# Performance work log

Measured on AMD Instinct MI355X. Metric: run time of the kernel, lower is better.

Reference implementation:

```python
import jax, jax.numpy as jnp
import numpy as np
import math

B, IN, OUT = 1024, 512, 512


def setup_inputs() -> dict:
    key = jax.random.key(0)
    ks = jax.random.split(key, 7)
    std = 1.0 / math.sqrt(IN)
    x = jax.random.normal(ks[0], (B, IN), dtype=jnp.float32)
    base_weight = jax.random.uniform(ks[1], (OUT, IN), dtype=jnp.float32, minval=-std, maxval=std)
    chirplet_weights = jax.random.uniform(ks[2], (OUT, IN), dtype=jnp.float32, minval=-std, maxval=std)
    # scale init ones, frequency ones, translation zeros; add small jitter for a non-degenerate test point
    scale = 1.0 + 0.1 * jax.random.normal(ks[3], (OUT, IN), dtype=jnp.float32)
    translation = 0.1 * jax.random.normal(ks[4], (OUT, IN), dtype=jnp.float32)
    frequency = 1.0 + 0.1 * jax.random.normal(ks[5], (OUT, IN), dtype=jnp.float32)
    bias = jax.random.uniform(ks[6], (OUT,), dtype=jnp.float32, minval=-std, maxval=std)
    return {"x": x, "base_weight": base_weight, "chirplet_weights": chirplet_weights,
            "scale": scale, "translation": translation, "frequency": frequency, "bias": bias}


def reference(x, base_weight, chirplet_weights, scale, translation, frequency, bias):
    TWO_PI = 2.0 * math.pi
    # base linear path: SiLU(x) @ W^T
    base_out = jnp.einsum('bi,oi->bo', jax.nn.silu(x), base_weight)
    # chirplet path: (b, o, i) intermediate reduced over i
    x_scaled = (x[:, None, :] - translation[None, :, :]) / scale[None, :, :]  # (B, OUT, IN)
    chirplet = jnp.cos(TWO_PI * frequency[None, :, :] * x_scaled) * jnp.exp(-0.5 * x_scaled ** 2)
    chirplet_out = jnp.einsum('boi,oi->bo', chirplet, chirplet_weights)
    return base_out + chirplet_out + bias[None, :]
```

## Files before the change

kernel.cpp:

```cpp
#include <hip/hip_runtime.h>
#include <hip/hip_bf16.h>

#define B_ 1024
#define IN_ 512
#define OUT_ 512
#define BTILE 64
#define OTILE 32
#define ITILE 8
#define KSPLIT 16
#define KCHUNK (IN_ / KSPLIT)
#define NCHUNKS (KCHUNK / ITILE)
#define P4STRIDE 128
#define PLSTRIDE 32
#define XSTRIDE 68
#define ASTRIDE 40

typedef float v2f   __attribute__((ext_vector_type(2)));
typedef float f32x4 __attribute__((ext_vector_type(4)));
typedef short s16x8 __attribute__((ext_vector_type(8)));
#define PKFMA(a, b, c) __builtin_elementwise_fma((v2f)(a), (v2f)(b), (v2f)(c))

__device__ __forceinline__ unsigned short f2bf(float f) {
    union { float f; unsigned int u; } v; v.f = f;
    unsigned int b = v.u + 0x7FFFu + ((v.u >> 16) & 1u);
    return (unsigned short)(b >> 16);
}
__device__ __forceinline__ float fast_exp2(float x) {
#if __has_builtin(__builtin_amdgcn_exp2f)
    return __builtin_amdgcn_exp2f(x);
#else
    return __exp2f(x);
#endif
}
__device__ __forceinline__ float fast_log2(float x) {
#if __has_builtin(__builtin_amdgcn_logf)
    return __builtin_amdgcn_logf(x);
#else
    return __log2f(x);
#endif
}
__device__ __forceinline__ float fast_cos_rev(float x) {
#if __has_builtin(__builtin_amdgcn_cosf)
    return __builtin_amdgcn_cosf(x);
#else
    return __cosf(x * 6.2831853071795864f);
#endif
}
__device__ __forceinline__ float fast_rcp(float x) {
#if __has_builtin(__builtin_amdgcn_rcpf)
    return __builtin_amdgcn_rcpf(x);
#else
    return 1.0f / x;
#endif
}

__global__ __launch_bounds__(256, 8) void chirplet_kernel(
    const float* __restrict__ x,
    const float* __restrict__ W,
    const float* __restrict__ Wc,
    const float* __restrict__ S,
    const float* __restrict__ T,
    const float* __restrict__ F,
    const float* __restrict__ bias,
    float* __restrict__ out)
{
    __shared__ __align__(16) float p4_lds[ITILE * P4STRIDE];
    __shared__ __align__(16) float plw_lds[ITILE * PLSTRIDE];
    __shared__ __align__(16) float x_lds[ITILE * XSTRIDE];
    __shared__ __align__(16) unsigned short sA_lds[BTILE * ASTRIDE];
    __shared__ __align__(16) unsigned short wB_lds[OTILE * ASTRIDE];

    const int tid  = threadIdx.x;
    const int wave = tid >> 6;
    const int lane = tid & 63;
    const int o0 = blockIdx.x * OTILE;
    const int b0 = blockIdx.y * BTILE;
    const int k0 = blockIdx.z * KCHUNK;

    const int oc = tid & 15;
    const int bq = tid >> 4;

    const int xrow = tid >> 2;
    const int xq   = tid & 3;

    const int pol = tid & 31;
    const int pi  = tid >> 5;

    const float LOG2E = 1.4426950408889634f;
    const float GK    = 0.8493218002880191f;

    v2f acc2[2][2] = {{{0.f,0.f},{0.f,0.f}},{{0.f,0.f},{0.f,0.f}}};

    for (int c = 0; c < NCHUNKS; ++c) {
        const int ib = k0 + c * ITILE;

        {
            const float2 v = *(const float2*)(x + (size_t)(b0 + xrow) * IN_ + ib + xq * 2);
            const float xf[2] = { v.x, v.y };
            unsigned int packed = 0;
            #pragma unroll
            for (int j = 0; j < 2; ++j) {
                const int col = xq * 2 + j;
                float xv  = xf[j];
                float sig = fast_rcp(1.0f + fast_exp2(-xv * LOG2E));
                x_lds[col * XSTRIDE + xrow] = xv;
                packed |= (unsigned int)f2bf(xv * sig) << (16 * j);
            }
            *(unsigned int*)&sA_lds[xrow * ASTRIDE + c * 8 + xq * 2] = packed;
        }

        {
            const size_t go = (size_t)(o0 + pol) * IN_ + ib + pi;
            const float s  = S[go];
            const float t  = T[go];
            const float f  = F[go];
            const float w  = W[go];
            const float wc = Wc[go];
            const float rs = fast_rcp(s);
            const float a  = f * rs;
            float4 p0;
            p0.x = a;
            p0.y = -a * t + (wc < 0.0f ? 0.5f : 0.0f);
            p0.z = rs * GK;
            p0.w = -t * rs * GK;
            *(float4*)&p4_lds[pi * P4STRIDE + pol * 4] = p0;
            plw_lds[pi * PLSTRIDE + pol] = fast_log2(fabsf(wc));
            wB_lds[pol * ASTRIDE + c * 8 + pi] = f2bf(w);
        }
        __syncthreads();

        #pragma unroll 4
        for (int i = 0; i < ITILE; ++i) {
            const float4 abcd[2] = {
                *(const float4*)&p4_lds[i * P4STRIDE + oc * 4],
                *(const float4*)&p4_lds[i * P4STRIDE + (oc + 16) * 4] };
            const float lw[2] = {
                plw_lds[i * PLSTRIDE + oc],
                plw_lds[i * PLSTRIDE + oc + 16] };
            const v2f* xp = (const v2f*)&x_lds[i * XSTRIDE + bq * 4];
            const v2f xk2[2] = { xp[0], xp[1] };
            #pragma unroll
            for (int o = 0; o < 2; ++o) {
                const v2f aa = { abcd[o].x, abcd[o].x };
                const v2f bb = { abcd[o].y, abcd[o].y };
                const v2f cc = { abcd[o].z, abcd[o].z };
                const v2f dd = { abcd[o].w, abcd[o].w };
                const v2f lwv = { lw[o], lw[o] };
                #pragma unroll
                for (int p = 0; p < 2; ++p) {
                    v2f rev = PKFMA(aa, xk2[p], bb);
                    v2f u   = PKFMA(cc, xk2[p], dd);
                    v2f arg = PKFMA(-u, u, lwv);
                    v2f co, e;
                    co.x = fast_cos_rev(rev.x);
                    co.y = fast_cos_rev(rev.y);
                    e.x  = fast_exp2(arg.x);
                    e.y  = fast_exp2(arg.y);
                    acc2[o][p] = PKFMA(co, e, acc2[o][p]);
                }
            }
        }
        __syncthreads();
    }

    const int q8 = (lane >> 4) * 8;
    const s16x8 af  = *(const s16x8*)&sA_lds[(wave * 16 + (lane & 15)) * ASTRIDE + q8];
    const s16x8 bf0 = *(const s16x8*)&wB_lds[(lane & 15) * ASTRIDE + q8];
    const s16x8 bf1 = *(const s16x8*)&wB_lds[((lane & 15) + 16) * ASTRIDE + q8];
    const f32x4 mz = { 0.f, 0.f, 0.f, 0.f };
    const f32x4 m0 = __builtin_amdgcn_mfma_f32_16x16x32_bf16(af, bf0, mz, 0, 0, 0);
    const f32x4 m1 = __builtin_amdgcn_mfma_f32_16x16x32_bf16(af, bf1, mz, 0, 0, 0);

    const float badd[2] = { (blockIdx.z == 0) ? bias[o0 + oc] : 0.0f,
                            (blockIdx.z == 0) ? bias[o0 + oc + 16] : 0.0f };
    #pragma unroll
    for (int o = 0; o < 2; ++o) {
        #pragma unroll
        for (int p = 0; p < 2; ++p) {
            #pragma unroll
            for (int j = 0; j < 2; ++j) {
                const int reg = p * 2 + j;
                const int b = b0 + bq * 4 + reg;
                float* dst = &out[(size_t)b * OUT_ + o0 + oc + o * 16];
                const float mm = (o == 0) ? m0[reg] : m1[reg];
                const float val = (j == 0 ? acc2[o][p].x : acc2[o][p].y) + mm + badd[o];
#if defined(__HIP_DEVICE_COMPILE__)
                unsafeAtomicAdd(dst, val);
#else
                atomicAdd(dst, val);
#endif
            }
        }
    }
}

extern "C" void kernel_launch(void* const* d_in, const int* in_sizes, int n_in,
                              void* d_out, int out_size, void* d_ws, size_t ws_size,
                              hipStream_t stream) {
    const float* x    = (const float*)d_in[0];
    const float* W    = (const float*)d_in[1];
    const float* Wc   = (const float*)d_in[2];
    const float* S    = (const float*)d_in[3];
    const float* T    = (const float*)d_in[4];
    const float* F    = (const float*)d_in[5];
    const float* bias = (const float*)d_in[6];
    float* out = (float*)d_out;

    hipMemsetAsync(out, 0, (size_t)out_size * sizeof(float), stream);

    dim3 grid(OUT_ / OTILE, B_ / BTILE, KSPLIT);
    chirplet_kernel<<<grid, 256, 0, stream>>>(x, W, Wc, S, T, F, bias, out);
}
```

Baseline: 125.9 us.

## Shrink blocks to 128 threads, halve K-split, accumulate MFMA per chunk

Blocks shrink from 64x32 to 32x32 (batch x output) with 128 threads, and the K-split drops from 16 to 8, so each block walks twice as many input chunks. The base-path bf16 MFMA now runs once per 8-wide chunk into a running accumulator, with only the first 16 lanes loading data and the rest fed zeros. Parameter loads are widened to float2, and LDS row strides are padded. The aim is to halve the atomic adds to the output and reuse the parameter transforms across more of the batch. The cost is fewer, longer blocks and an MFMA issued with most of its K dimension padded with zeros on every chunk.

```diff
diff --git a/kernel.cpp b/kernel.cpp
--- a/kernel.cpp
+++ b/kernel.cpp
@@ -4,16 +4,17 @@
 #define B_ 1024
 #define IN_ 512
 #define OUT_ 512
-#define BTILE 64
+#define BTILE 32
 #define OTILE 32
 #define ITILE 8
-#define KSPLIT 16
+#define KSPLIT 8
 #define KCHUNK (IN_ / KSPLIT)
 #define NCHUNKS (KCHUNK / ITILE)
-#define P4STRIDE 128
-#define PLSTRIDE 32
-#define XSTRIDE 68
-#define ASTRIDE 40
+#define THREADS 128
+#define P4ROW 132
+#define PLROW 33
+#define XSTRIDE 36
+#define SASTRIDE 8
 
 typedef float v2f   __attribute__((ext_vector_type(2)));
 typedef float f32x4 __attribute__((ext_vector_type(4)));
@@ -54,7 +55,7 @@
 #endif
 }
 
-__global__ __launch_bounds__(256, 8) void chirplet_kernel(
+__global__ __launch_bounds__(THREADS, 8) void chirplet_kernel(
     const float* __restrict__ x,
     const float* __restrict__ W,
     const float* __restrict__ Wc,
@@ -64,11 +65,11 @@
     const float* __restrict__ bias,
     float* __restrict__ out)
 {
-    __shared__ __align__(16) float p4_lds[ITILE * P4STRIDE];
-    __shared__ __align__(16) float plw_lds[ITILE * PLSTRIDE];
+    __shared__ __align__(16) float p4_lds[ITILE * P4ROW];
+    __shared__ __align__(16) float plw_lds[ITILE * PLROW];
     __shared__ __align__(16) float x_lds[ITILE * XSTRIDE];
-    __shared__ __align__(16) unsigned short sA_lds[BTILE * ASTRIDE];
-    __shared__ __align__(16) unsigned short wB_lds[OTILE * ASTRIDE];
+    __shared__ __align__(16) unsigned short sA_lds[BTILE * SASTRIDE];
+    __shared__ __align__(16) unsigned short wB_lds[OTILE * SASTRIDE];
 
     const int tid  = threadIdx.x;
     const int wave = tid >> 6;
@@ -77,68 +78,93 @@
     const int b0 = blockIdx.y * BTILE;
     const int k0 = blockIdx.z * KCHUNK;
 
-    const int oc = tid & 15;
-    const int bq = tid >> 4;
-
-    const int xrow = tid >> 2;
-    const int xq   = tid & 3;
-
-    const int pol = tid & 31;
-    const int pi  = tid >> 5;
+    const int oc = lane & 15;
+    const int lq = lane >> 4;
+    const int xb = wave * 16 + lq * 4;
+
+    const int xr = tid >> 2;
+    const int xq = tid & 3;
+
+    const int po = tid & 31;
+    const int ph = tid >> 5;
 
     const float LOG2E = 1.4426950408889634f;
     const float GK    = 0.8493218002880191f;
 
     v2f acc2[2][2] = {{{0.f,0.f},{0.f,0.f}},{{0.f,0.f},{0.f,0.f}}};
+    f32x4 accg[2] = {{0.f,0.f,0.f,0.f},{0.f,0.f,0.f,0.f}};
 
     for (int c = 0; c < NCHUNKS; ++c) {
         const int ib = k0 + c * ITILE;
 
         {
-            const float2 v = *(const float2*)(x + (size_t)(b0 + xrow) * IN_ + ib + xq * 2);
+            const float2 v = *(const float2*)(x + (size_t)(b0 + xr) * IN_ + ib + xq * 2);
             const float xf[2] = { v.x, v.y };
             unsigned int packed = 0;
             #pragma unroll
             for (int j = 0; j < 2; ++j) {
                 const int col = xq * 2 + j;
-                float xv  = xf[j];
-                float sig = fast_rcp(1.0f + fast_exp2(-xv * LOG2E));
-                x_lds[col * XSTRIDE + xrow] = xv;
+                const float xv  = xf[j];
+                const float sig = fast_rcp(1.0f + fast_exp2(-xv * LOG2E));
+                x_lds[col * XSTRIDE + xr] = xv;
                 packed |= (unsigned int)f2bf(xv * sig) << (16 * j);
             }
-            *(unsigned int*)&sA_lds[xrow * ASTRIDE + c * 8 + xq * 2] = packed;
+            *(unsigned int*)&sA_lds[xr * SASTRIDE + xq * 2] = packed;
         }
 
         {
-            const size_t go = (size_t)(o0 + pol) * IN_ + ib + pi;
-            const float s  = S[go];
-            const float t  = T[go];
-            const float f  = F[go];
-            const float w  = W[go];
-            const float wc = Wc[go];
-            const float rs = fast_rcp(s);
-            const float a  = f * rs;
-            float4 p0;
-            p0.x = a;
-            p0.y = -a * t + (wc < 0.0f ? 0.5f : 0.0f);
-            p0.z = rs * GK;
-            p0.w = -t * rs * GK;
-            *(float4*)&p4_lds[pi * P4STRIDE + pol * 4] = p0;
-            plw_lds[pi * PLSTRIDE + pol] = fast_log2(fabsf(wc));
-            wB_lds[pol * ASTRIDE + c * 8 + pi] = f2bf(w);
+            const size_t go = (size_t)(o0 + po) * IN_ + ib + ph * 2;
+            const float2 s2  = *(const float2*)(S + go);
+            const float2 t2  = *(const float2*)(T + go);
+            const float2 f2  = *(const float2*)(F + go);
+            const float2 wc2 = *(const float2*)(Wc + go);
+            const float2 w2  = *(const float2*)(W + go);
+            const float sA[2]  = { s2.x, s2.y };
+            const float tA[2]  = { t2.x, t2.y };
+            const float fA[2]  = { f2.x, f2.y };
+            const float wcA[2] = { wc2.x, wc2.y };
+            unsigned int wpk = 0;
+            #pragma unroll
+            for (int j = 0; j < 2; ++j) {
+                const int slot = ph * 2 + j;
+                const float rs = fast_rcp(sA[j]);
+                const float a  = fA[j] * rs;
+                float4 p0;
+                p0.x = a;
+                p0.y = -a * tA[j] + (wcA[j] < 0.0f ? 0.5f : 0.0f);
+                p0.z = rs * GK;
+                p0.w = -tA[j] * rs * GK;
+                *(float4*)&p4_lds[slot * P4ROW + po * 4] = p0;
+                plw_lds[slot * PLROW + po] = fast_log2(fabsf(wcA[j]));
+                wpk |= (unsigned int)f2bf(j == 0 ? w2.x : w2.y) << (16 * j);
+            }
+            *(unsigned int*)&wB_lds[po * SASTRIDE + ph * 2] = wpk;
         }
         __syncthreads();
+
+        {
+            s16x8 af = {0,0,0,0,0,0,0,0}, bf0 = af, bf1 = af;
+            if (lane < 16) {
+                af  = *(const s16x8*)&sA_lds[(wave * 16 + (lane & 15)) * SASTRIDE];
+                bf0 = *(const s16x8*)&wB_lds[(lane & 15) * SASTRIDE];
+                bf1 = *(const s16x8*)&wB_lds[((lane & 15) + 16) * SASTRIDE];
+            }
+            accg[0] = __builtin_amdgcn_mfma_f32_16x16x32_bf16(af, bf0, accg[0], 0, 0, 0);
+            accg[1] = __builtin_amdgcn_mfma_f32_16x16x32_bf16(af, bf1, accg[1], 0, 0, 0);
+        }
 
         #pragma unroll 4
         for (int i = 0; i < ITILE; ++i) {
             const float4 abcd[2] = {
-                *(const float4*)&p4_lds[i * P4STRIDE + oc * 4],
-                *(const float4*)&p4_lds[i * P4STRIDE + (oc + 16) * 4] };
+                *(const float4*)&p4_lds[i * P4ROW + oc * 4],
+                *(const float4*)&p4_lds[i * P4ROW + (oc + 16) * 4] };
             const float lw[2] = {
-                plw_lds[i * PLSTRIDE + oc],
-                plw_lds[i * PLSTRIDE + oc + 16] };
-            const v2f* xp = (const v2f*)&x_lds[i * XSTRIDE + bq * 4];
-            const v2f xk2[2] = { xp[0], xp[1] };
+                plw_lds[i * PLROW + oc],
+                plw_lds[i * PLROW + oc + 16] };
+            const f32x4 xk4 = *(const f32x4*)&x_lds[i * XSTRIDE + xb];
+            const v2f xk2[2] = {
+                __builtin_shufflevector(xk4, xk4, 0, 1),
+                __builtin_shufflevector(xk4, xk4, 2, 3) };
             #pragma unroll
             for (int o = 0; o < 2; ++o) {
                 const v2f aa = { abcd[o].x, abcd[o].x };
@@ -163,14 +189,6 @@
         __syncthreads();
     }
 
-    const int q8 = (lane >> 4) * 8;
-    const s16x8 af  = *(const s16x8*)&sA_lds[(wave * 16 + (lane & 15)) * ASTRIDE + q8];
-    const s16x8 bf0 = *(const s16x8*)&wB_lds[(lane & 15) * ASTRIDE + q8];
-    const s16x8 bf1 = *(const s16x8*)&wB_lds[((lane & 15) + 16) * ASTRIDE + q8];
-    const f32x4 mz = { 0.f, 0.f, 0.f, 0.f };
-    const f32x4 m0 = __builtin_amdgcn_mfma_f32_16x16x32_bf16(af, bf0, mz, 0, 0, 0);
-    const f32x4 m1 = __builtin_amdgcn_mfma_f32_16x16x32_bf16(af, bf1, mz, 0, 0, 0);
-
     const float badd[2] = { (blockIdx.z == 0) ? bias[o0 + oc] : 0.0f,
                             (blockIdx.z == 0) ? bias[o0 + oc + 16] : 0.0f };
     #pragma unroll
@@ -180,10 +198,10 @@
             #pragma unroll
             for (int j = 0; j < 2; ++j) {
                 const int reg = p * 2 + j;
-                const int b = b0 + bq * 4 + reg;
+                const int b = b0 + wave * 16 + lq * 4 + reg;
                 float* dst = &out[(size_t)b * OUT_ + o0 + oc + o * 16];
-                const float mm = (o == 0) ? m0[reg] : m1[reg];
-                const float val = (j == 0 ? acc2[o][p].x : acc2[o][p].y) + mm + badd[o];
+                const float val = (j == 0 ? acc2[o][p].x : acc2[o][p].y)
+                                + accg[o][reg] + badd[o];
 #if defined(__HIP_DEVICE_COMPILE__)
                 unsafeAtomicAdd(dst, val);
 #else
@@ -209,5 +227,5 @@
     hipMemsetAsync(out, 0, (size_t)out_size * sizeof(float), stream);
 
     dim3 grid(OUT_ / OTILE, B_ / BTILE, KSPLIT);
-    chirplet_kernel<<<grid, 256, 0, stream>>>(x, W, Wc, S, T, F, bias, out);
-}
+    chirplet_kernel<<<grid, THREADS, 0, stream>>>(x, W, Wc, S, T, F, bias, out);
+}
```

Result: slower. 133.8 us (+6.3%).
